# Optimization experiments

Hardware: AMD Instinct MI355X
Metric: run time of the kernel (lower is better)

The kernel has to match this reference:

```python
import jax, jax.numpy as jnp
import numpy as np

N = 100000      # nodes
E = 1600000     # edges (before self-loops)
F_IN = 128
H = 4           # heads, layer 1
C = 32          # hidden_size (per-head channels)
G = 256         # graphs in batch
NEG_SLOPE = 0.2 # PyG GATConv default


def setup_inputs() -> dict:
    key = jax.random.key(0)
    ks = jax.random.split(key, 12)
    x = jax.random.normal(ks[0], (N, F_IN), jnp.float32)
    edge_index = jax.random.randint(ks[1], (2, E), 0, N, dtype=jnp.int64)
    batch = jnp.sort(jax.random.randint(ks[2], (N,), 0, G, dtype=jnp.int64))
    s = lambda f: np.float32(1.0 / np.sqrt(f))
    W1 = jax.random.normal(ks[3], (F_IN, H * C), jnp.float32) * s(F_IN)
    att_src1 = jax.random.normal(ks[4], (H, C), jnp.float32) * 0.1
    att_dst1 = jax.random.normal(ks[5], (H, C), jnp.float32) * 0.1
    b1 = jnp.zeros((H * C,), jnp.float32)
    W2 = jax.random.normal(ks[6], (H * C, C), jnp.float32) * s(H * C)
    att_src2 = jax.random.normal(ks[7], (1, C), jnp.float32) * 0.1
    att_dst2 = jax.random.normal(ks[8], (1, C), jnp.float32) * 0.1
    b2 = jnp.zeros((C,), jnp.float32)
    Wfc = jax.random.normal(ks[9], (C, 1), jnp.float32) * s(C)
    bfc = jnp.zeros((1,), jnp.float32)
    return {"x": x, "edge_index": edge_index, "batch": batch,
            "W1": W1, "att_src1": att_src1, "att_dst1": att_dst1, "b1": b1,
            "W2": W2, "att_src2": att_src2, "att_dst2": att_dst2, "b2": b2,
            "Wfc": Wfc, "bfc": bfc}


def gat_conv(x, src, dst, W, att_s, att_d, b, heads, ch):
    """PyG GATConv (concat=True): linear, per-head additive attention,
    segment softmax over destination nodes, scatter-add aggregation."""
    n = x.shape[0]
    h = (x @ W).reshape(n, heads, ch)                         # [N,H,C]
    a_s = jnp.einsum('nhc,hc->nh', h, att_s)                  # [N,H]
    a_d = jnp.einsum('nhc,hc->nh', h, att_d)                  # [N,H]
    e = jax.nn.leaky_relu(a_s[src] + a_d[dst], NEG_SLOPE)     # [E,H]
    m = jax.ops.segment_max(e, dst, num_segments=n)           # stable softmax
    e = jnp.exp(e - m[dst])
    denom = jax.ops.segment_sum(e, dst, num_segments=n)
    alpha = e / denom[dst]                                    # [E,H]
    out = jax.ops.segment_sum(h[src] * alpha[:, :, None], dst, num_segments=n)
    return out.reshape(n, heads * ch) + b


def reference(x, edge_index, batch, W1, att_src1, att_dst1, b1,
              W2, att_src2, att_dst2, b2, Wfc, bfc):
    n = x.shape[0]
    loops = jnp.arange(n, dtype=edge_index.dtype)             # PyG add_self_loops=True
    src = jnp.concatenate([edge_index[0], loops])
    dst = jnp.concatenate([edge_index[1], loops])
    h = jax.nn.relu(gat_conv(x, src, dst, W1, att_src1, att_dst1, b1, H, C))
    h = jax.nn.relu(gat_conv(h, src, dst, W2, att_src2, att_dst2, b2, 1, C))
    # global_mean_pool over ragged graph segments
    sums = jax.ops.segment_sum(h, batch, num_segments=G)      # [G,C]
    cnts = jax.ops.segment_sum(jnp.ones((n,), h.dtype), batch, num_segments=G)
    pooled = sums / jnp.maximum(cnts, 1.0)[:, None]
    return (pooled @ Wfc + bfc).squeeze(-1)                   # [G]
```

## Files before the change

### kernel.cpp

```cpp
#include <hip/hip_runtime.h>
#include <cmath>

#define NEG_SLOPE 0.2f
#define DPB 128
#define EPB 4096

typedef unsigned int uint32;
typedef unsigned short ushort16;
typedef unsigned char uchar8;
typedef __attribute__((ext_vector_type(8))) short bf16x8;
typedef __attribute__((ext_vector_type(4))) float f32x4;
typedef __attribute__((ext_vector_type(2))) float f32x2;

__device__ __forceinline__ ushort16 f2bf(float x) {
    uint32 b = __float_as_uint(x);
    b += 0x7FFFu + ((b >> 16) & 1u);
    return (ushort16)(b >> 16);
}
__device__ __forceinline__ float bf2f_lo(uint32 u) { return __uint_as_float(u << 16); }
__device__ __forceinline__ float bf2f_hi(uint32 u) { return __uint_as_float(u & 0xFFFF0000u); }

__global__ void prep_B1(const float* __restrict__ W1, const float* __restrict__ atts,
                        const float* __restrict__ attd, ushort16* __restrict__ Bt) {
    int idx = blockIdx.x * 256 + threadIdx.x;
    if (idx >= 144 * 128) return;
    int n = idx >> 7, k = idx & 127;
    float v = 0.f;
    if (n < 128) v = W1[k * 128 + n];
    else if (n < 132) { int h = n - 128; for (int c = 0; c < 32; c++) v += W1[k*128 + h*32 + c] * atts[h*32 + c]; }
    else if (n < 136) { int h = n - 132; for (int c = 0; c < 32; c++) v += W1[k*128 + h*32 + c] * attd[h*32 + c]; }
    Bt[idx] = f2bf(v);
}
__global__ void prep_B2(const float* __restrict__ W2, const float* __restrict__ atts,
                        const float* __restrict__ attd, ushort16* __restrict__ Bt) {
    int idx = blockIdx.x * 256 + threadIdx.x;
    if (idx >= 48 * 128) return;
    int n = idx >> 7, k = idx & 127;
    float v = 0.f;
    if (n < 32) v = W2[k * 32 + n];
    else if (n == 32) { for (int c = 0; c < 32; c++) v += W2[k*32 + c] * atts[c]; }
    else if (n == 33) { for (int c = 0; c < 32; c++) v += W2[k*32 + c] * attd[c]; }
    Bt[idx] = f2bf(v);
}

template<int NT, int NH, bool XBF, bool OUT8>
__global__ __launch_bounds__(256) void gemm_mfma(
    const void* __restrict__ Xv, const ushort16* __restrict__ Bt,
    void* __restrict__ Houtv, float* __restrict__ asd, int M)
{
    constexpr int HT = NT - 1;
    constexpr int KP = 136;
    __shared__ ushort16 Bl[NT * 16 * KP];
    const int t = threadIdx.x;
    for (int i = t; i < NT * 16 * 32; i += 256) {
        int n = i >> 5, k4 = i & 31;
        uint2 v = *(const uint2*)&Bt[n * 128 + k4 * 4];
        *(uint2*)&Bl[n * KP + k4 * 4] = v;
    }
    __syncthreads();
    const int wave = t >> 6, lane = t & 63;
    const int lrow = lane & 15, lgrp = lane >> 4;
    const int ntiles = (M + 127) >> 7;
    const float* Xf = (const float*)Xv;
    const ushort16* Xb = (const ushort16*)Xv;

    for (int tile = blockIdx.x; tile < ntiles; tile += gridDim.x) {
        const int rbase = tile * 128 + wave * 32;
        f32x4 acc[2][NT];
        #pragma unroll
        for (int rs = 0; rs < 2; rs++)
            #pragma unroll
            for (int n = 0; n < NT; n++) acc[rs][n] = (f32x4){0.f, 0.f, 0.f, 0.f};

        for (int kk = 0; kk < 4; kk++) {
            bf16x8 bf[NT];
            #pragma unroll
            for (int n = 0; n < NT; n++)
                bf[n] = *(const bf16x8*)&Bl[(n * 16 + lrow) * KP + kk * 32 + lgrp * 8];
            #pragma unroll
            for (int rs = 0; rs < 2; rs++) {
                int row = rbase + rs * 16 + lrow;
                int rowc = row < M ? row : M - 1;
                bf16x8 af;
                if constexpr (XBF) {
                    af = *(const bf16x8*)&Xb[(long)rowc * 128 + kk * 32 + lgrp * 8];
                } else {
                    const float* xp = Xf + (long)rowc * 128 + kk * 32 + lgrp * 8;
                    float4 f0 = *(const float4*)xp;
                    float4 f1 = *(const float4*)(xp + 4);
                    union { uint32 u[4]; bf16x8 v; } pk;
                    pk.u[0] = (uint32)f2bf(f0.x) | ((uint32)f2bf(f0.y) << 16);
                    pk.u[1] = (uint32)f2bf(f0.z) | ((uint32)f2bf(f0.w) << 16);
                    pk.u[2] = (uint32)f2bf(f1.x) | ((uint32)f2bf(f1.y) << 16);
                    pk.u[3] = (uint32)f2bf(f1.z) | ((uint32)f2bf(f1.w) << 16);
                    af = pk.v;
                }
                #pragma unroll
                for (int n = 0; n < NT; n++)
                    acc[rs][n] = __builtin_amdgcn_mfma_f32_16x16x32_bf16(af, bf[n], acc[rs][n], 0, 0, 0);
            }
        }
        #pragma unroll
        for (int rs = 0; rs < 2; rs++) {
            #pragma unroll
            for (int r = 0; r < 4; r++) {
                const int row = rbase + rs * 16 + lgrp * 4 + r;
                if (row < M) {
                    if constexpr (OUT8) {
                        uchar8* H8 = (uchar8*)Houtv;
                        #pragma unroll
                        for (int n = 0; n < HT; n++) {
                            int pk = __builtin_amdgcn_cvt_pk_fp8_f32(acc[rs][n][r], 0.f, 0, false);
                            H8[(long)row * (HT * 16) + n * 16 + lrow] = (uchar8)pk;
                        }
                    } else {
                        ushort16* Hh = (ushort16*)Houtv;
                        #pragma unroll
                        for (int n = 0; n < HT; n++)
                            Hh[(long)row * (HT * 16) + n * 16 + lrow] = f2bf(acc[rs][n][r]);
                    }
                    if (lrow < 2 * NH)
                        asd[(long)row * (2 * NH) + lrow] = acc[rs][NT - 1][r];
                }
            }
        }
    }
}

__global__ __launch_bounds__(256) void buck_hist_k(
    const int* __restrict__ ei, int E, int Etot,
    int* __restrict__ cnt_bb, int NBUK_, int NBLK_)
{
    __shared__ int hist[1024];
    const int b = blockIdx.x, t = threadIdx.x;
    for (int i = t; i < NBUK_; i += 256) hist[i] = 0;
    __syncthreads();
    const int e0 = b * EPB;
    for (int i = t; i < EPB; i += 256) {
        int e = e0 + i;
        if (e < Etot) {
            int d = (e < E) ? ei[E + e] : (e - E);
            atomicAdd(&hist[d >> 7], 1);
        }
    }
    __syncthreads();
    for (int i = t; i < NBUK_; i += 256) cnt_bb[(size_t)i * NBLK_ + b] = hist[i];
}

__global__ __launch_bounds__(256) void buck_scan_row_k(
    int* __restrict__ cnt_bb, int* __restrict__ rowTot, int NBLK_)
{
    __shared__ int tmp[256];
    const int k = blockIdx.x, t = threadIdx.x;
    int* row = cnt_bb + (size_t)k * NBLK_;
    const int base = t * 4;
    int v[4]; int s = 0;
    #pragma unroll
    for (int j = 0; j < 4; j++) { v[j] = (base + j < NBLK_) ? row[base + j] : 0; s += v[j]; }
    tmp[t] = s; __syncthreads();
    for (int off = 1; off < 256; off <<= 1) {
        int x = (t >= off) ? tmp[t - off] : 0;
        __syncthreads();
        tmp[t] += x;
        __syncthreads();
    }
    int run = tmp[t] - s;
    if (t == 255) rowTot[k] = tmp[255];
    #pragma unroll
    for (int j = 0; j < 4; j++) { if (base + j < NBLK_) row[base + j] = run; run += v[j]; }
}

__global__ __launch_bounds__(256) void buck_base_k(
    const int* __restrict__ rowTot, int* __restrict__ bucketBase, int NBUK_)
{
    __shared__ int tmp[256];
    const int t = threadIdx.x;
    const int base = t * 4;
    int v[4]; int s = 0;
    #pragma unroll
    for (int j = 0; j < 4; j++) {
        v[j] = (base + j < NBUK_) ? ((rowTot[base + j] + 3 * DPB + 7) & ~7) : 0;
        s += v[j];
    }
    tmp[t] = s; __syncthreads();
    for (int off = 1; off < 256; off <<= 1) {
        int x = (t >= off) ? tmp[t - off] : 0;
        __syncthreads();
        tmp[t] += x;
        __syncthreads();
    }
    int run = tmp[t] - s;
    #pragma unroll
    for (int j = 0; j < 4; j++) { if (base + j < NBUK_) bucketBase[base + j] = run; run += v[j]; }
}

__global__ __launch_bounds__(256) void buck_scatter_k(
    const int* __restrict__ ei, int E, int Etot,
    const int* __restrict__ cnt_bb, const int* __restrict__ bucketBase,
    uint32* __restrict__ be, int NBUK_, int NBLK_)
{
    __shared__ int cur[1024];
    const int b = blockIdx.x, t = threadIdx.x;
    for (int i = t; i < NBUK_; i += 256)
        cur[i] = bucketBase[i] + cnt_bb[(size_t)i * NBLK_ + b];
    __syncthreads();
    const int e0 = b * EPB;
    for (int i = t; i < EPB; i += 256) {
        int e = e0 + i;
        if (e < Etot) {
            int srcv, d;
            if (e < E) { srcv = ei[e]; d = ei[E + e]; } else { srcv = d = e - E; }
            int slot = atomicAdd(&cur[d >> 7], 1);
            be[slot] = (uint32)srcv | ((uint32)(d & (DPB - 1)) << 20);
        }
    }
}

__global__ __launch_bounds__(256) void buck_finalize_k(
    const uint32* __restrict__ be, const int* __restrict__ rowTot,
    const int* __restrict__ bucketBase,
    int* __restrict__ csr, int* __restrict__ indptr, int* __restrict__ count, int N_)
{
    __shared__ int lhist[DPB];
    __shared__ int lptr[DPB];
    __shared__ int lcur[DPB];
    __shared__ int stmp[DPB];
    __shared__ int img[6144];
    __shared__ int paddedTotS;
    const int k = blockIdx.x, t = threadIdx.x;
    const int baseG = bucketBase[k];
    const int Mk = rowTot[k];
    if (t < DPB) lhist[t] = 0;
    __syncthreads();
    for (int i = t; i < Mk; i += 256) atomicAdd(&lhist[be[baseG + i] >> 20], 1);
    __syncthreads();
    int myp = (t < DPB) ? ((lhist[t] + 3) & ~3) : 0;
    if (t < DPB) stmp[t] = myp;
    __syncthreads();
    for (int off = 1; off < DPB; off <<= 1) {
        int x = (t < DPB && t >= off) ? stmp[t - off] : 0;
        __syncthreads();
        if (t < DPB) stmp[t] += x;
        __syncthreads();
    }
    if (t < DPB) { lptr[t] = stmp[t] - myp; lcur[t] = stmp[t] - myp; }
    if (t == DPB - 1) paddedTotS = stmp[t];
    __syncthreads();
    const int paddedTot = paddedTotS < 6144 ? paddedTotS : 6144;
    for (int i = t; i < paddedTot; i += 256) img[i] = 0;
    if (t < DPB) {
        int d = k * DPB + t;
        if (d < N_) { count[d] = lhist[t]; indptr[d] = baseG + lptr[t]; }
    }
    __syncthreads();
    for (int i = t; i < Mk; i += 256) {
        uint32 pk = be[baseG + i];
        int slot = atomicAdd(&lcur[pk >> 20], 1);
        if (slot < 6144) img[slot] = (int)(pk & 0xFFFFFu);
    }
    __syncthreads();
    for (int i = t; i < paddedTot; i += 256) csr[baseG + i] = img[i];
}

__global__ __launch_bounds__(256) void edge_p_k(
    const int* __restrict__ csr, const int* __restrict__ indptr, const int* __restrict__ count,
    const float* __restrict__ asd, ushort16* __restrict__ p1h, int N, int EP)
{
    int wave = threadIdx.x >> 6, lane = threadIdx.x & 63;
    int dst = blockIdx.x * 4 + wave;
    if (dst >= N) return;
    const char* asdb = (const char*)asd;
    const int start = indptr[dst], cnt = count[dst];
    const int cntp = (cnt + 3) & ~3;
    const float4 ad = *(const float4*)(asdb + (((uint32)dst << 5) | 16u));
    for (int k = lane; k < cntp; k += 64) {
        ushort16 r0 = 0, r1 = 0, r2 = 0, r3 = 0;
        if (k < cnt) {
            uint32 s = (uint32)csr[start + k];
            float4 as = *(const float4*)(asdb + (s << 5));
            float e0 = as.x + ad.x, e1 = as.y + ad.y, e2 = as.z + ad.z, e3 = as.w + ad.w;
            e0 = e0 >= 0.f ? e0 : NEG_SLOPE * e0;
            e1 = e1 >= 0.f ? e1 : NEG_SLOPE * e1;
            e2 = e2 >= 0.f ? e2 : NEG_SLOPE * e2;
            e3 = e3 >= 0.f ? e3 : NEG_SLOPE * e3;
            r0 = f2bf(__expf(e0)); r1 = f2bf(__expf(e1));
            r2 = f2bf(__expf(e2)); r3 = f2bf(__expf(e3));
        }
        const int pos = start + k;
        p1h[pos] = r0;
        p1h[EP + pos] = r1;
        p1h[2 * EP + pos] = r2;
        p1h[3 * EP + pos] = r3;
    }
}

__global__ __launch_bounds__(256) void edge_p2_k(
    const int* __restrict__ csr, const int* __restrict__ indptr, const int* __restrict__ count,
    const float* __restrict__ asd2, ushort16* __restrict__ p2, int N)
{
    int wave = threadIdx.x >> 6, lane = threadIdx.x & 63;
    int dst = blockIdx.x * 4 + wave;
    if (dst >= N) return;
    const char* asdb = (const char*)asd2;
    const int start = indptr[dst], cnt = count[dst];
    const int cntp = (cnt + 3) & ~3;
    const float ad = *(const float*)(asdb + (((uint32)dst << 3) | 4u));
    for (int k = lane; k < cntp; k += 64) {
        ushort16 r = 0;
        if (k < cnt) {
            uint32 s = (uint32)csr[start + k];
            float el = *(const float*)(asdb + (s << 3)) + ad;
            el = el >= 0.f ? el : NEG_SLOPE * el;
            r = f2bf(__expf(el));
        }
        p2[start + k] = r;
    }
}

__global__ __launch_bounds__(256) void agg_flash_h4(
    const int* __restrict__ csr, const ushort16* __restrict__ p1h,
    const int* __restrict__ indptr, const int* __restrict__ count,
    const uchar8* __restrict__ H8, const float* __restrict__ b1,
    uint32* __restrict__ Out, int N, int EP)
{
    int wave = threadIdx.x >> 6, lane = threadIdx.x & 63;
    int dst = blockIdx.x * 4 + wave;
    if (dst >= N) return;
    const char* Hb = (const char*)H8;
    const int head = lane >> 4;
    const uint32 ch2 = (uint32)(lane * 2);
    const int start = indptr[dst], cnt = count[dst];
    const int cntp = (cnt + 3) & ~3;
    const ushort16* pp = p1h + (size_t)head * EP + start;
    float s = 0.f, a0 = 0.f, a1 = 0.f;
    int k = 0;
    for (; k + 8 <= cntp; k += 8) {
        const int4 svA = *(const int4*)&csr[start + k];
        const int4 svB = *(const int4*)&csr[start + k + 4];
        const uint2 pwA = *(const uint2*)&pp[k];
        const uint2 pwB = *(const uint2*)&pp[k + 4];
        const uint32 u0 = *(const ushort16*)(Hb + (((uint32)svA.x << 7) | ch2));
        const uint32 u1 = *(const ushort16*)(Hb + (((uint32)svA.y << 7) | ch2));
        const uint32 u2 = *(const ushort16*)(Hb + (((uint32)svA.z << 7) | ch2));
        const uint32 u3 = *(const ushort16*)(Hb + (((uint32)svA.w << 7) | ch2));
        const uint32 u4 = *(const ushort16*)(Hb + (((uint32)svB.x << 7) | ch2));
        const uint32 u5 = *(const ushort16*)(Hb + (((uint32)svB.y << 7) | ch2));
        const uint32 u6 = *(const ushort16*)(Hb + (((uint32)svB.z << 7) | ch2));
        const uint32 u7 = *(const ushort16*)(Hb + (((uint32)svB.w << 7) | ch2));
        const f32x2 h0 = __builtin_amdgcn_cvt_pk_f32_fp8((int)u0, false);
        const f32x2 h1 = __builtin_amdgcn_cvt_pk_f32_fp8((int)u1, false);
        const f32x2 h2 = __builtin_amdgcn_cvt_pk_f32_fp8((int)u2, false);
        const f32x2 h3 = __builtin_amdgcn_cvt_pk_f32_fp8((int)u3, false);
        const f32x2 h4 = __builtin_amdgcn_cvt_pk_f32_fp8((int)u4, false);
        const f32x2 h5 = __builtin_amdgcn_cvt_pk_f32_fp8((int)u5, false);
        const f32x2 h6 = __builtin_amdgcn_cvt_pk_f32_fp8((int)u6, false);
        const f32x2 h7 = __builtin_amdgcn_cvt_pk_f32_fp8((int)u7, false);
        const float p0 = bf2f_lo(pwA.x), p1v = bf2f_hi(pwA.x);
        const float p2v = bf2f_lo(pwA.y), p3v = bf2f_hi(pwA.y);
        const float p4v = bf2f_lo(pwB.x), p5v = bf2f_hi(pwB.x);
        const float p6v = bf2f_lo(pwB.y), p7v = bf2f_hi(pwB.y);
        s += ((p0 + p1v) + (p2v + p3v)) + ((p4v + p5v) + (p6v + p7v));
        a0 += p0 * h0[0];  a1 += p0 * h0[1];
        a0 += p1v * h1[0]; a1 += p1v * h1[1];
        a0 += p2v * h2[0]; a1 += p2v * h2[1];
        a0 += p3v * h3[0]; a1 += p3v * h3[1];
        a0 += p4v * h4[0]; a1 += p4v * h4[1];
        a0 += p5v * h5[0]; a1 += p5v * h5[1];
        a0 += p6v * h6[0]; a1 += p6v * h6[1];
        a0 += p7v * h7[0]; a1 += p7v * h7[1];
    }
    if (k < cntp) {
        const int4 sv = *(const int4*)&csr[start + k];
        const uint2 pw = *(const uint2*)&pp[k];
        const uint32 u0 = *(const ushort16*)(Hb + (((uint32)sv.x << 7) | ch2));
        const uint32 u1 = *(const ushort16*)(Hb + (((uint32)sv.y << 7) | ch2));
        const uint32 u2 = *(const ushort16*)(Hb + (((uint32)sv.z << 7) | ch2));
        const uint32 u3 = *(const ushort16*)(Hb + (((uint32)sv.w << 7) | ch2));
        const f32x2 h0 = __builtin_amdgcn_cvt_pk_f32_fp8((int)u0, false);
        const f32x2 h1 = __builtin_amdgcn_cvt_pk_f32_fp8((int)u1, false);
        const f32x2 h2 = __builtin_amdgcn_cvt_pk_f32_fp8((int)u2, false);
        const f32x2 h3 = __builtin_amdgcn_cvt_pk_f32_fp8((int)u3, false);
        const float p0 = bf2f_lo(pw.x), p1v = bf2f_hi(pw.x);
        const float p2v = bf2f_lo(pw.y), p3v = bf2f_hi(pw.y);
        s += (p0 + p1v) + (p2v + p3v);
        a0 += p0 * h0[0];  a1 += p0 * h0[1];
        a0 += p1v * h1[0]; a1 += p1v * h1[1];
        a0 += p2v * h2[0]; a1 += p2v * h2[1];
        a0 += p3v * h3[0]; a1 += p3v * h3[1];
    }
    const float inv = 1.f / s;
    const float2 bb = *(const float2*)&b1[ch2];
    float o0 = fmaxf(a0 * inv + bb.x, 0.f);
    float o1 = fmaxf(a1 * inv + bb.y, 0.f);
    Out[(long)dst * 64 + lane] = (uint32)f2bf(o0) | ((uint32)f2bf(o1) << 16);
}

__global__ __launch_bounds__(256) void agg_flash_h1(
    const int* __restrict__ csr, const ushort16* __restrict__ p2,
    const int* __restrict__ indptr, const int* __restrict__ count,
    const uchar8* __restrict__ H8, float* __restrict__ Out, int N)
{
    int wave = threadIdx.x >> 6, lane = threadIdx.x & 63;
    int dst = blockIdx.x * 4 + wave;
    if (dst >= N) return;
    const char* Hb = (const char*)H8;
    const int c2 = lane & 15, grp = lane >> 4;
    const uint32 cb = (uint32)(c2 * 2);
    const int start = indptr[dst];
    const int cntp = (count[dst] + 3) & ~3;
    float s = 0.f, a0 = 0.f, a1 = 0.f;
    for (int k = grp * 4; k < cntp; k += 16) {
        const int4  sv = *(const int4*)&csr[start + k];
        const uint2 pv = *(const uint2*)&p2[start + k];
        const uint32 u0 = *(const ushort16*)(Hb + (((uint32)sv.x << 5) | cb));
        const uint32 u1 = *(const ushort16*)(Hb + (((uint32)sv.y << 5) | cb));
        const uint32 u2 = *(const ushort16*)(Hb + (((uint32)sv.z << 5) | cb));
        const uint32 u3 = *(const ushort16*)(Hb + (((uint32)sv.w << 5) | cb));
        const f32x2 h0 = __builtin_amdgcn_cvt_pk_f32_fp8((int)u0, false);
        const f32x2 h1 = __builtin_amdgcn_cvt_pk_f32_fp8((int)u1, false);
        const f32x2 h2 = __builtin_amdgcn_cvt_pk_f32_fp8((int)u2, false);
        const f32x2 h3 = __builtin_amdgcn_cvt_pk_f32_fp8((int)u3, false);
        float q0 = bf2f_lo(pv.x), q1 = bf2f_hi(pv.x);
        float q2 = bf2f_lo(pv.y), q3 = bf2f_hi(pv.y);
        s += (q0 + q1) + (q2 + q3);
        a0 += q0 * h0[0]; a1 += q0 * h0[1];
        a0 += q1 * h1[0]; a1 += q1 * h1[1];
        a0 += q2 * h2[0]; a1 += q2 * h2[1];
        a0 += q3 * h3[0]; a1 += q3 * h3[1];
    }
    s  += __shfl_xor(s, 16, 64);  s  += __shfl_xor(s, 32, 64);
    a0 += __shfl_xor(a0, 16, 64); a0 += __shfl_xor(a0, 32, 64);
    a1 += __shfl_xor(a1, 16, 64); a1 += __shfl_xor(a1, 32, 64);
    if (grp == 0) {
        const float inv = 1.f / s;
        float2 o; o.x = a0 * inv; o.y = a1 * inv;
        *(float2*)&Out[(long)dst * 32 + c2 * 2] = o;
    }
}

__global__ __launch_bounds__(256) void pool_fc_kernel(
    const float* __restrict__ Agg2, const float* __restrict__ b2,
    const int* __restrict__ batch,
    const float* __restrict__ Wfc, const float* __restrict__ bfc,
    float* __restrict__ out, int N)
{
    __shared__ float part[8][32];
    const int g = blockIdx.x;
    const int t = threadIdx.x;
    const int c = t & 31, grp = t >> 5;

    int lo = 0, hi = N;
    while (lo < hi) { int mid = (lo + hi) >> 1; if (batch[mid] < g) lo = mid + 1; else hi = mid; }
    const int start = lo;
    hi = N;
    while (lo < hi) { int mid = (lo + hi) >> 1; if (batch[mid] <= g) lo = mid + 1; else hi = mid; }
    const int end = lo;

    const float bc = b2[c];
    float acc = 0.f;
    for (int i = start + grp; i < end; i += 8)
        acc += fmaxf(Agg2[(long)i * 32 + c] + bc, 0.f);
    part[grp][c] = acc;
    __syncthreads();
    if (t < 32) {
        float s = 0.f;
        #pragma unroll
        for (int r = 0; r < 8; r++) s += part[r][c];
        const float cnt = fmaxf((float)(end - start), 1.f);
        float v = (s / cnt) * Wfc[c];
        #pragma unroll
        for (int m = 16; m >= 1; m >>= 1) v += __shfl_xor(v, m, 64);
        if (c == 0) out[g] = v + bfc[0];
    }
}

extern "C" void kernel_launch(void* const* d_in, const int* in_sizes, int n_in,
                              void* d_out, int out_size, void* d_ws, size_t ws_size,
                              hipStream_t stream)
{
    const float* x     = (const float*)d_in[0];
    const int*   ei    = (const int*)d_in[1];
    const int*   batch = (const int*)d_in[2];
    const float* W1    = (const float*)d_in[3];
    const float* atts1 = (const float*)d_in[4];
    const float* attd1 = (const float*)d_in[5];
    const float* b1    = (const float*)d_in[6];
    const float* W2    = (const float*)d_in[7];
    const float* atts2 = (const float*)d_in[8];
    const float* attd2 = (const float*)d_in[9];
    const float* b2    = (const float*)d_in[10];
    const float* Wfc   = (const float*)d_in[11];
    const float* bfc   = (const float*)d_in[12];
    float* out = (float*)d_out;

    const int N = in_sizes[0] / 128;
    const int E = in_sizes[1] / 2;
    const int Etot = E + N;
    const int G = out_size;
    const int NBUK = (N + DPB - 1) / DPB;
    const int NBLK = (Etot + EPB - 1) / EPB;
    const int CSRCAP = (Etot + NBUK * (3 * DPB + 8) + 7) & ~7;
    const int ntiles = (N + 127) >> 7;

    float* w = (float*)d_ws;
    uchar8* h1   = (uchar8*)w; w += (size_t)N * 32;
    uchar8* h2   = (uchar8*)w; w += (size_t)N * 8;
    uint32* agg1 = (uint32*)w; w += (size_t)N * 64;
    float* agg2 = w; w += (size_t)N * 32;
    float* asd1 = w; w += (size_t)N * 8;
    float* asd2 = w; w += (size_t)N * 2;
    ushort16* Bt1 = (ushort16*)w; w += (144 * 128) / 2;
    ushort16* Bt2 = (ushort16*)w; w += (48 * 128) / 2;
    int* count  = (int*)w; w += N;
    int* indptr = (int*)w; w += N;
    int* cnt_bb = (int*)w; w += (size_t)NBUK * NBLK;
    int* rowTot = (int*)w; w += NBUK;
    int* bucketBase = (int*)w; w += NBUK;
    uint32* be  = (uint32*)w; w += CSRCAP;
    int* csr    = (int*)w; w += CSRCAP;
    ushort16* p1h = (ushort16*)w; w += (size_t)CSRCAP * 2;
    ushort16* p2  = (ushort16*)w; w += CSRCAP / 2;

    prep_B1<<<(144 * 128 + 255) / 256, 256, 0, stream>>>(W1, atts1, attd1, Bt1);
    prep_B2<<<(48 * 128 + 255) / 256, 256, 0, stream>>>(W2, atts2, attd2, Bt2);

    gemm_mfma<9, 4, false, true><<<ntiles, 256, 0, stream>>>(x, Bt1, h1, asd1, N);

    buck_hist_k<<<NBLK, 256, 0, stream>>>(ei, E, Etot, cnt_bb, NBUK, NBLK);
    buck_scan_row_k<<<NBUK, 256, 0, stream>>>(cnt_bb, rowTot, NBLK);
    buck_base_k<<<1, 256, 0, stream>>>(rowTot, bucketBase, NBUK);
    buck_scatter_k<<<NBLK, 256, 0, stream>>>(ei, E, Etot, cnt_bb, bucketBase, be, NBUK, NBLK);
    buck_finalize_k<<<NBUK, 256, 0, stream>>>(be, rowTot, bucketBase, csr, indptr, count, N);

    edge_p_k<<<(N + 3) / 4, 256, 0, stream>>>(csr, indptr, count, asd1, p1h, N, CSRCAP);
    agg_flash_h4<<<(N + 3) / 4, 256, 0, stream>>>(csr, p1h, indptr, count, h1, b1, agg1, N, CSRCAP);

    gemm_mfma<3, 1, true, true><<<ntiles, 256, 0, stream>>>(agg1, Bt2, h2, asd2, N);
    edge_p2_k<<<(N + 3) / 4, 256, 0, stream>>>(csr, indptr, count, asd2, p2, N);
    agg_flash_h1<<<(N + 3) / 4, 256, 0, stream>>>(csr, p2, indptr, count, h2, agg2, N);

    pool_fc_kernel<<<G, 256, 0, stream>>>(agg2, b2, batch, Wfc, bfc, out, N);
}
```

Before: 242.2 us.

## Pre-shift CSR indices, pad rows to 8, widen aggregation loads to 4 fp8 channels

The CSR entries now store the source index already shifted to a byte offset, so the gathers no longer need a per-edge shift. Per-destination padding goes from 4 to 8 so both aggregation kernels can split each row's edges across two lane halves (h4) or eight groups (h1). Each lane now loads 4 fp8 channels per gather instead of 2, halving the number of gather instructions, and the partial sums are combined with a cross-lane reduction. The two weight-prep kernels are also merged into one launch. In exchange the padding overhead and CSR capacity grow, and the h4 kernel gains a cross-lane reduction step.

```diff
diff --git a/kernel.cpp b/kernel.cpp
--- a/kernel.cpp
+++ b/kernel.cpp
@@ -20,27 +20,29 @@
 __device__ __forceinline__ float bf2f_lo(uint32 u) { return __uint_as_float(u << 16); }
 __device__ __forceinline__ float bf2f_hi(uint32 u) { return __uint_as_float(u & 0xFFFF0000u); }
 
-__global__ void prep_B1(const float* __restrict__ W1, const float* __restrict__ atts,
-                        const float* __restrict__ attd, ushort16* __restrict__ Bt) {
+__global__ void prep_B(const float* __restrict__ W1, const float* __restrict__ atts1,
+                       const float* __restrict__ attd1,
+                       const float* __restrict__ W2, const float* __restrict__ atts2,
+                       const float* __restrict__ attd2,
+                       ushort16* __restrict__ Bt1, ushort16* __restrict__ Bt2) {
     int idx = blockIdx.x * 256 + threadIdx.x;
-    if (idx >= 144 * 128) return;
-    int n = idx >> 7, k = idx & 127;
-    float v = 0.f;
-    if (n < 128) v = W1[k * 128 + n];
-    else if (n < 132) { int h = n - 128; for (int c = 0; c < 32; c++) v += W1[k*128 + h*32 + c] * atts[h*32 + c]; }
-    else if (n < 136) { int h = n - 132; for (int c = 0; c < 32; c++) v += W1[k*128 + h*32 + c] * attd[h*32 + c]; }
-    Bt[idx] = f2bf(v);
-}
-__global__ void prep_B2(const float* __restrict__ W2, const float* __restrict__ atts,
-                        const float* __restrict__ attd, ushort16* __restrict__ Bt) {
-    int idx = blockIdx.x * 256 + threadIdx.x;
-    if (idx >= 48 * 128) return;
-    int n = idx >> 7, k = idx & 127;
-    float v = 0.f;
-    if (n < 32) v = W2[k * 32 + n];
-    else if (n == 32) { for (int c = 0; c < 32; c++) v += W2[k*32 + c] * atts[c]; }
-    else if (n == 33) { for (int c = 0; c < 32; c++) v += W2[k*32 + c] * attd[c]; }
-    Bt[idx] = f2bf(v);
+    if (idx < 144 * 128) {
+        int n = idx >> 7, k = idx & 127;
+        float v = 0.f;
+        if (n < 128) v = W1[k * 128 + n];
+        else if (n < 132) { int h = n - 128; for (int c = 0; c < 32; c++) v += W1[k*128 + h*32 + c] * atts1[h*32 + c]; }
+        else if (n < 136) { int h = n - 132; for (int c = 0; c < 32; c++) v += W1[k*128 + h*32 + c] * attd1[h*32 + c]; }
+        Bt1[idx] = f2bf(v);
+    } else {
+        int j = idx - 144 * 128;
+        if (j >= 48 * 128) return;
+        int n = j >> 7, k = j & 127;
+        float v = 0.f;
+        if (n < 32) v = W2[k * 32 + n];
+        else if (n == 32) { for (int c = 0; c < 32; c++) v += W2[k*32 + c] * atts2[c]; }
+        else if (n == 33) { for (int c = 0; c < 32; c++) v += W2[k*32 + c] * attd2[c]; }
+        Bt2[j] = f2bf(v);
+    }
 }
 
 template<int NT, int NH, bool XBF, bool OUT8>
@@ -179,7 +181,7 @@
     int v[4]; int s = 0;
     #pragma unroll
     for (int j = 0; j < 4; j++) {
-        v[j] = (base + j < NBUK_) ? ((rowTot[base + j] + 3 * DPB + 7) & ~7) : 0;
+        v[j] = (base + j < NBUK_) ? ((rowTot[base + j] + 7 * DPB + 7) & ~7) : 0;
         s += v[j];
     }
     tmp[t] = s; __syncthreads();
@@ -234,7 +236,7 @@
     __syncthreads();
     for (int i = t; i < Mk; i += 256) atomicAdd(&lhist[be[baseG + i] >> 20], 1);
     __syncthreads();
-    int myp = (t < DPB) ? ((lhist[t] + 3) & ~3) : 0;
+    int myp = (t < DPB) ? ((lhist[t] + 7) & ~7) : 0;
     if (t < DPB) stmp[t] = myp;
     __syncthreads();
     for (int off = 1; off < DPB; off <<= 1) {
@@ -256,7 +258,7 @@
     for (int i = t; i < Mk; i += 256) {
         uint32 pk = be[baseG + i];
         int slot = atomicAdd(&lcur[pk >> 20], 1);
-        if (slot < 6144) img[slot] = (int)(pk & 0xFFFFFu);
+        if (slot < 6144) img[slot] = (int)((pk & 0xFFFFFu) << 7);
     }
     __syncthreads();
     for (int i = t; i < paddedTot; i += 256) csr[baseG + i] = img[i];
@@ -271,13 +273,13 @@
     if (dst >= N) return;
     const char* asdb = (const char*)asd;
     const int start = indptr[dst], cnt = count[dst];
-    const int cntp = (cnt + 3) & ~3;
+    const int cntp = (cnt + 7) & ~7;
     const float4 ad = *(const float4*)(asdb + (((uint32)dst << 5) | 16u));
     for (int k = lane; k < cntp; k += 64) {
         ushort16 r0 = 0, r1 = 0, r2 = 0, r3 = 0;
         if (k < cnt) {
-            uint32 s = (uint32)csr[start + k];
-            float4 as = *(const float4*)(asdb + (s << 5));
+            uint32 sb = (uint32)csr[start + k];
+            float4 as = *(const float4*)(asdb + (sb >> 2));
             float e0 = as.x + ad.x, e1 = as.y + ad.y, e2 = as.z + ad.z, e3 = as.w + ad.w;
             e0 = e0 >= 0.f ? e0 : NEG_SLOPE * e0;
             e1 = e1 >= 0.f ? e1 : NEG_SLOPE * e1;
@@ -303,13 +305,13 @@
     if (dst >= N) return;
     const char* asdb = (const char*)asd2;
     const int start = indptr[dst], cnt = count[dst];
-    const int cntp = (cnt + 3) & ~3;
+    const int cntp = (cnt + 7) & ~7;
     const float ad = *(const float*)(asdb + (((uint32)dst << 3) | 4u));
     for (int k = lane; k < cntp; k += 64) {
         ushort16 r = 0;
         if (k < cnt) {
-            uint32 s = (uint32)csr[start + k];
-            float el = *(const float*)(asdb + (s << 3)) + ad;
+            uint32 sb = (uint32)csr[start + k];
+            float el = *(const float*)(asdb + (sb >> 4)) + ad;
             el = el >= 0.f ? el : NEG_SLOPE * el;
             r = f2bf(__expf(el));
         }
@@ -327,72 +329,54 @@
     int dst = blockIdx.x * 4 + wave;
     if (dst >= N) return;
     const char* Hb = (const char*)H8;
-    const int head = lane >> 4;
-    const uint32 ch2 = (uint32)(lane * 2);
+    const int l32 = lane & 31, half = lane >> 5;
+    const int head = l32 >> 3;
+    const uint32 cb = (uint32)(l32 * 4);
     const int start = indptr[dst], cnt = count[dst];
-    const int cntp = (cnt + 3) & ~3;
-    const ushort16* pp = p1h + (size_t)head * EP + start;
-    float s = 0.f, a0 = 0.f, a1 = 0.f;
-    int k = 0;
-    for (; k + 8 <= cntp; k += 8) {
-        const int4 svA = *(const int4*)&csr[start + k];
-        const int4 svB = *(const int4*)&csr[start + k + 4];
-        const uint2 pwA = *(const uint2*)&pp[k];
-        const uint2 pwB = *(const uint2*)&pp[k + 4];
-        const uint32 u0 = *(const ushort16*)(Hb + (((uint32)svA.x << 7) | ch2));
-        const uint32 u1 = *(const ushort16*)(Hb + (((uint32)svA.y << 7) | ch2));
-        const uint32 u2 = *(const ushort16*)(Hb + (((uint32)svA.z << 7) | ch2));
-        const uint32 u3 = *(const ushort16*)(Hb + (((uint32)svA.w << 7) | ch2));
-        const uint32 u4 = *(const ushort16*)(Hb + (((uint32)svB.x << 7) | ch2));
-        const uint32 u5 = *(const ushort16*)(Hb + (((uint32)svB.y << 7) | ch2));
-        const uint32 u6 = *(const ushort16*)(Hb + (((uint32)svB.z << 7) | ch2));
-        const uint32 u7 = *(const ushort16*)(Hb + (((uint32)svB.w << 7) | ch2));
-        const f32x2 h0 = __builtin_amdgcn_cvt_pk_f32_fp8((int)u0, false);
-        const f32x2 h1 = __builtin_amdgcn_cvt_pk_f32_fp8((int)u1, false);
-        const f32x2 h2 = __builtin_amdgcn_cvt_pk_f32_fp8((int)u2, false);
-        const f32x2 h3 = __builtin_amdgcn_cvt_pk_f32_fp8((int)u3, false);
-        const f32x2 h4 = __builtin_amdgcn_cvt_pk_f32_fp8((int)u4, false);
-        const f32x2 h5 = __builtin_amdgcn_cvt_pk_f32_fp8((int)u5, false);
-        const f32x2 h6 = __builtin_amdgcn_cvt_pk_f32_fp8((int)u6, false);
-        const f32x2 h7 = __builtin_amdgcn_cvt_pk_f32_fp8((int)u7, false);
-        const float p0 = bf2f_lo(pwA.x), p1v = bf2f_hi(pwA.x);
-        const float p2v = bf2f_lo(pwA.y), p3v = bf2f_hi(pwA.y);
-        const float p4v = bf2f_lo(pwB.x), p5v = bf2f_hi(pwB.x);
-        const float p6v = bf2f_lo(pwB.y), p7v = bf2f_hi(pwB.y);
-        s += ((p0 + p1v) + (p2v + p3v)) + ((p4v + p5v) + (p6v + p7v));
-        a0 += p0 * h0[0];  a1 += p0 * h0[1];
-        a0 += p1v * h1[0]; a1 += p1v * h1[1];
-        a0 += p2v * h2[0]; a1 += p2v * h2[1];
-        a0 += p3v * h3[0]; a1 += p3v * h3[1];
-        a0 += p4v * h4[0]; a1 += p4v * h4[1];
-        a0 += p5v * h5[0]; a1 += p5v * h5[1];
-        a0 += p6v * h6[0]; a1 += p6v * h6[1];
-        a0 += p7v * h7[0]; a1 += p7v * h7[1];
-    }
-    if (k < cntp) {
-        const int4 sv = *(const int4*)&csr[start + k];
+    const int cntp = (cnt + 7) & ~7;
+    const int* cp = csr + start + half * 4;
+    const ushort16* pp = p1h + (size_t)head * EP + start + half * 4;
+    float s = 0.f, a0 = 0.f, a1 = 0.f, a2 = 0.f, a3 = 0.f;
+    for (int k = 0; k < cntp; k += 8) {
+        const int4 sv = *(const int4*)&cp[k];
         const uint2 pw = *(const uint2*)&pp[k];
-        const uint32 u0 = *(const ushort16*)(Hb + (((uint32)sv.x << 7) | ch2));
-        const uint32 u1 = *(const ushort16*)(Hb + (((uint32)sv.y << 7) | ch2));
-        const uint32 u2 = *(const ushort16*)(Hb + (((uint32)sv.z << 7) | ch2));
-        const uint32 u3 = *(const ushort16*)(Hb + (((uint32)sv.w << 7) | ch2));
-        const f32x2 h0 = __builtin_amdgcn_cvt_pk_f32_fp8((int)u0, false);
-        const f32x2 h1 = __builtin_amdgcn_cvt_pk_f32_fp8((int)u1, false);
-        const f32x2 h2 = __builtin_amdgcn_cvt_pk_f32_fp8((int)u2, false);
-        const f32x2 h3 = __builtin_amdgcn_cvt_pk_f32_fp8((int)u3, false);
+        const uint32 u0 = *(const uint32*)(Hb + ((uint32)sv.x | cb));
+        const uint32 u1 = *(const uint32*)(Hb + ((uint32)sv.y | cb));
+        const uint32 u2 = *(const uint32*)(Hb + ((uint32)sv.z | cb));
+        const uint32 u3 = *(const uint32*)(Hb + ((uint32)sv.w | cb));
+        const f32x2 l0 = __builtin_amdgcn_cvt_pk_f32_fp8((int)u0, false);
+        const f32x2 g0 = __builtin_amdgcn_cvt_pk_f32_fp8((int)u0, true);
+        const f32x2 l1 = __builtin_amdgcn_cvt_pk_f32_fp8((int)u1, false);
+        const f32x2 g1 = __builtin_amdgcn_cvt_pk_f32_fp8((int)u1, true);
+        const f32x2 l2 = __builtin_amdgcn_cvt_pk_f32_fp8((int)u2, false);
+        const f32x2 g2 = __builtin_amdgcn_cvt_pk_f32_fp8((int)u2, true);
+        const f32x2 l3 = __builtin_amdgcn_cvt_pk_f32_fp8((int)u3, false);
+        const f32x2 g3 = __builtin_amdgcn_cvt_pk_f32_fp8((int)u3, true);
         const float p0 = bf2f_lo(pw.x), p1v = bf2f_hi(pw.x);
         const float p2v = bf2f_lo(pw.y), p3v = bf2f_hi(pw.y);
         s += (p0 + p1v) + (p2v + p3v);
-        a0 += p0 * h0[0];  a1 += p0 * h0[1];
-        a0 += p1v * h1[0]; a1 += p1v * h1[1];
-        a0 += p2v * h2[0]; a1 += p2v * h2[1];
-        a0 += p3v * h3[0]; a1 += p3v * h3[1];
-    }
-    const float inv = 1.f / s;
-    const float2 bb = *(const float2*)&b1[ch2];
-    float o0 = fmaxf(a0 * inv + bb.x, 0.f);
-    float o1 = fmaxf(a1 * inv + bb.y, 0.f);
-    Out[(long)dst * 64 + lane] = (uint32)f2bf(o0) | ((uint32)f2bf(o1) << 16);
+        a0 += p0 * l0[0];  a1 += p0 * l0[1];  a2 += p0 * g0[0];  a3 += p0 * g0[1];
+        a0 += p1v * l1[0]; a1 += p1v * l1[1]; a2 += p1v * g1[0]; a3 += p1v * g1[1];
+        a0 += p2v * l2[0]; a1 += p2v * l2[1]; a2 += p2v * g2[0]; a3 += p2v * g2[1];
+        a0 += p3v * l3[0]; a1 += p3v * l3[1]; a2 += p3v * g3[0]; a3 += p3v * g3[1];
+    }
+    s  += __shfl_xor(s, 32, 64);
+    a0 += __shfl_xor(a0, 32, 64);
+    a1 += __shfl_xor(a1, 32, 64);
+    a2 += __shfl_xor(a2, 32, 64);
+    a3 += __shfl_xor(a3, 32, 64);
+    if (half == 0) {
+        const float inv = 1.f / s;
+        const float4 bb = *(const float4*)&b1[l32 * 4];
+        float o0 = fmaxf(a0 * inv + bb.x, 0.f);
+        float o1 = fmaxf(a1 * inv + bb.y, 0.f);
+        float o2 = fmaxf(a2 * inv + bb.z, 0.f);
+        float o3 = fmaxf(a3 * inv + bb.w, 0.f);
+        uint2 o;
+        o.x = (uint32)f2bf(o0) | ((uint32)f2bf(o1) << 16);
+        o.y = (uint32)f2bf(o2) | ((uint32)f2bf(o3) << 16);
+        *(uint2*)&Out[(long)dst * 64 + l32 * 2] = o;
+    }
 }
 
 __global__ __launch_bounds__(256) void agg_flash_h1(
@@ -404,37 +388,46 @@
     int dst = blockIdx.x * 4 + wave;
     if (dst >= N) return;
     const char* Hb = (const char*)H8;
-    const int c2 = lane & 15, grp = lane >> 4;
-    const uint32 cb = (uint32)(c2 * 2);
+    const int c4 = lane & 7, grp = lane >> 3;
+    const uint32 cb = (uint32)(c4 * 4);
     const int start = indptr[dst];
-    const int cntp = (count[dst] + 3) & ~3;
-    float s = 0.f, a0 = 0.f, a1 = 0.f;
-    for (int k = grp * 4; k < cntp; k += 16) {
+    const int cntp = (count[dst] + 7) & ~7;
+    float s = 0.f, a0 = 0.f, a1 = 0.f, a2 = 0.f, a3 = 0.f;
+    for (int k = grp * 4; k < cntp; k += 32) {
         const int4  sv = *(const int4*)&csr[start + k];
         const uint2 pv = *(const uint2*)&p2[start + k];
-        const uint32 u0 = *(const ushort16*)(Hb + (((uint32)sv.x << 5) | cb));
-        const uint32 u1 = *(const ushort16*)(Hb + (((uint32)sv.y << 5) | cb));
-        const uint32 u2 = *(const ushort16*)(Hb + (((uint32)sv.z << 5) | cb));
-        const uint32 u3 = *(const ushort16*)(Hb + (((uint32)sv.w << 5) | cb));
-        const f32x2 h0 = __builtin_amdgcn_cvt_pk_f32_fp8((int)u0, false);
-        const f32x2 h1 = __builtin_amdgcn_cvt_pk_f32_fp8((int)u1, false);
-        const f32x2 h2 = __builtin_amdgcn_cvt_pk_f32_fp8((int)u2, false);
-        const f32x2 h3 = __builtin_amdgcn_cvt_pk_f32_fp8((int)u3, false);
+        const uint32 u0 = *(const uint32*)(Hb + (((uint32)sv.x >> 2) | cb));
+        const uint32 u1 = *(const uint32*)(Hb + (((uint32)sv.y >> 2) | cb));
+        const uint32 u2 = *(const uint32*)(Hb + (((uint32)sv.z >> 2) | cb));
+        const uint32 u3 = *(const uint32*)(Hb + (((uint32)sv.w >> 2) | cb));
+        const f32x2 l0 = __builtin_amdgcn_cvt_pk_f32_fp8((int)u0, false);
+        const f32x2 g0 = __builtin_amdgcn_cvt_pk_f32_fp8((int)u0, true);
+        const f32x2 l1 = __builtin_amdgcn_cvt_pk_f32_fp8((int)u1, false);
+        const f32x2 g1 = __builtin_amdgcn_cvt_pk_f32_fp8((int)u1, true);
+        const f32x2 l2 = __builtin_amdgcn_cvt_pk_f32_fp8((int)u2, false);
+        const f32x2 g2 = __builtin_amdgcn_cvt_pk_f32_fp8((int)u2, true);
+        const f32x2 l3 = __builtin_amdgcn_cvt_pk_f32_fp8((int)u3, false);
+        const f32x2 g3 = __builtin_amdgcn_cvt_pk_f32_fp8((int)u3, true);
         float q0 = bf2f_lo(pv.x), q1 = bf2f_hi(pv.x);
         float q2 = bf2f_lo(pv.y), q3 = bf2f_hi(pv.y);
         s += (q0 + q1) + (q2 + q3);
-        a0 += q0 * h0[0]; a1 += q0 * h0[1];
-        a0 += q1 * h1[0]; a1 += q1 * h1[1];
-        a0 += q2 * h2[0]; a1 += q2 * h2[1];
-        a0 += q3 * h3[0]; a1 += q3 * h3[1];
-    }
-    s  += __shfl_xor(s, 16, 64);  s  += __shfl_xor(s, 32, 64);
-    a0 += __shfl_xor(a0, 16, 64); a0 += __shfl_xor(a0, 32, 64);
-    a1 += __shfl_xor(a1, 16, 64); a1 += __shfl_xor(a1, 32, 64);
+        a0 += q0 * l0[0]; a1 += q0 * l0[1]; a2 += q0 * g0[0]; a3 += q0 * g0[1];
+        a0 += q1 * l1[0]; a1 += q1 * l1[1]; a2 += q1 * g1[0]; a3 += q1 * g1[1];
+        a0 += q2 * l2[0]; a1 += q2 * l2[1]; a2 += q2 * g2[0]; a3 += q2 * g2[1];
+        a0 += q3 * l3[0]; a1 += q3 * l3[1]; a2 += q3 * g3[0]; a3 += q3 * g3[1];
+    }
+    #pragma unroll
+    for (int m = 8; m <= 32; m <<= 1) {
+        s  += __shfl_xor(s, m, 64);
+        a0 += __shfl_xor(a0, m, 64);
+        a1 += __shfl_xor(a1, m, 64);
+        a2 += __shfl_xor(a2, m, 64);
+        a3 += __shfl_xor(a3, m, 64);
+    }
     if (grp == 0) {
         const float inv = 1.f / s;
-        float2 o; o.x = a0 * inv; o.y = a1 * inv;
-        *(float2*)&Out[(long)dst * 32 + c2 * 2] = o;
+        float4 o; o.x = a0 * inv; o.y = a1 * inv; o.z = a2 * inv; o.w = a3 * inv;
+        *(float4*)&Out[(long)dst * 32 + c4 * 4] = o;
     }
 }
 
@@ -499,7 +492,7 @@
     const int G = out_size;
     const int NBUK = (N + DPB - 1) / DPB;
     const int NBLK = (Etot + EPB - 1) / EPB;
-    const int CSRCAP = (Etot + NBUK * (3 * DPB + 8) + 7) & ~7;
+    const int CSRCAP = (Etot + NBUK * (7 * DPB + 8) + 7) & ~7;
     const int ntiles = (N + 127) >> 7;
 
     float* w = (float*)d_ws;
@@ -521,8 +514,7 @@
     ushort16* p1h = (ushort16*)w; w += (size_t)CSRCAP * 2;
     ushort16* p2  = (ushort16*)w; w += CSRCAP / 2;
 
-    prep_B1<<<(144 * 128 + 255) / 256, 256, 0, stream>>>(W1, atts1, attd1, Bt1);
-    prep_B2<<<(48 * 128 + 255) / 256, 256, 0, stream>>>(W2, atts2, attd2, Bt2);
+    prep_B<<<(192 * 128 + 255) / 256, 256, 0, stream>>>(W1, atts1, attd1, W2, atts2, attd2, Bt1, Bt2);
 
     gemm_mfma<9, 4, false, true><<<ntiles, 256, 0, stream>>>(x, Bt1, h1, asd1, N);
 
```

Measured after the change: 238.9 us. No clear change (-1.4%).

## Fuse layer-1 edge score computation into CSR finalize and pre-scale CSR indices

Applied to the files above, without the earlier changes.

Merges the two weight-prep kernels into one launch, and folds the layer-1 edge attention/exp computation into the bucket finalize kernel. The finalize kernel now keeps the destination of each slot in shared memory and caches the destination attention values, which removes a separate pass that re-read the CSR. CSR entries are stored pre-shifted (source index << 7) so the gather kernels skip a shift when forming addresses and use a right shift instead. This adds shared-memory use in finalize, which may lower occupancy, and limits how large source indices can be before the shifted value overflows.

```diff
diff --git a/kernel.cpp b/kernel.cpp
--- a/kernel.cpp
+++ b/kernel.cpp
@@ -20,27 +20,29 @@
 __device__ __forceinline__ float bf2f_lo(uint32 u) { return __uint_as_float(u << 16); }
 __device__ __forceinline__ float bf2f_hi(uint32 u) { return __uint_as_float(u & 0xFFFF0000u); }
 
-__global__ void prep_B1(const float* __restrict__ W1, const float* __restrict__ atts,
-                        const float* __restrict__ attd, ushort16* __restrict__ Bt) {
+__global__ void prep_B(const float* __restrict__ W1, const float* __restrict__ atts1,
+                       const float* __restrict__ attd1,
+                       const float* __restrict__ W2, const float* __restrict__ atts2,
+                       const float* __restrict__ attd2,
+                       ushort16* __restrict__ Bt1, ushort16* __restrict__ Bt2) {
     int idx = blockIdx.x * 256 + threadIdx.x;
-    if (idx >= 144 * 128) return;
-    int n = idx >> 7, k = idx & 127;
-    float v = 0.f;
-    if (n < 128) v = W1[k * 128 + n];
-    else if (n < 132) { int h = n - 128; for (int c = 0; c < 32; c++) v += W1[k*128 + h*32 + c] * atts[h*32 + c]; }
-    else if (n < 136) { int h = n - 132; for (int c = 0; c < 32; c++) v += W1[k*128 + h*32 + c] * attd[h*32 + c]; }
-    Bt[idx] = f2bf(v);
-}
-__global__ void prep_B2(const float* __restrict__ W2, const float* __restrict__ atts,
-                        const float* __restrict__ attd, ushort16* __restrict__ Bt) {
-    int idx = blockIdx.x * 256 + threadIdx.x;
-    if (idx >= 48 * 128) return;
-    int n = idx >> 7, k = idx & 127;
-    float v = 0.f;
-    if (n < 32) v = W2[k * 32 + n];
-    else if (n == 32) { for (int c = 0; c < 32; c++) v += W2[k*32 + c] * atts[c]; }
-    else if (n == 33) { for (int c = 0; c < 32; c++) v += W2[k*32 + c] * attd[c]; }
-    Bt[idx] = f2bf(v);
+    if (idx < 144 * 128) {
+        int n = idx >> 7, k = idx & 127;
+        float v = 0.f;
+        if (n < 128) v = W1[k * 128 + n];
+        else if (n < 132) { int h = n - 128; for (int c = 0; c < 32; c++) v += W1[k*128 + h*32 + c] * atts1[h*32 + c]; }
+        else if (n < 136) { int h = n - 132; for (int c = 0; c < 32; c++) v += W1[k*128 + h*32 + c] * attd1[h*32 + c]; }
+        Bt1[idx] = f2bf(v);
+    } else {
+        int j = idx - 144 * 128;
+        if (j >= 48 * 128) return;
+        int n = j >> 7, k = j & 127;
+        float v = 0.f;
+        if (n < 32) v = W2[k * 32 + n];
+        else if (n == 32) { for (int c = 0; c < 32; c++) v += W2[k*32 + c] * atts2[c]; }
+        else if (n == 33) { for (int c = 0; c < 32; c++) v += W2[k*32 + c] * attd2[c]; }
+        Bt2[j] = f2bf(v);
+    }
 }
 
 template<int NT, int NH, bool XBF, bool OUT8>
@@ -218,14 +220,17 @@
 
 __global__ __launch_bounds__(256) void buck_finalize_k(
     const uint32* __restrict__ be, const int* __restrict__ rowTot,
-    const int* __restrict__ bucketBase,
-    int* __restrict__ csr, int* __restrict__ indptr, int* __restrict__ count, int N_)
+    const int* __restrict__ bucketBase, const float* __restrict__ asd1,
+    int* __restrict__ csr, int* __restrict__ indptr, int* __restrict__ count,
+    ushort16* __restrict__ p1h, int N_, int EP)
 {
     __shared__ int lhist[DPB];
     __shared__ int lptr[DPB];
     __shared__ int lcur[DPB];
     __shared__ int stmp[DPB];
     __shared__ int img[6144];
+    __shared__ short slot2d[6144];
+    __shared__ float4 adl[DPB];
     __shared__ int paddedTotS;
     const int k = blockIdx.x, t = threadIdx.x;
     const int baseG = bucketBase[k];
@@ -247,37 +252,35 @@
     if (t == DPB - 1) paddedTotS = stmp[t];
     __syncthreads();
     const int paddedTot = paddedTotS < 6144 ? paddedTotS : 6144;
-    for (int i = t; i < paddedTot; i += 256) img[i] = 0;
+    for (int i = t; i < paddedTot; i += 256) { img[i] = 0; slot2d[i] = -1; }
     if (t < DPB) {
         int d = k * DPB + t;
-        if (d < N_) { count[d] = lhist[t]; indptr[d] = baseG + lptr[t]; }
+        if (d < N_) {
+            count[d] = lhist[t];
+            indptr[d] = baseG + lptr[t];
+            adl[t] = *(const float4*)&asd1[(size_t)d * 8 + 4];
+        }
     }
     __syncthreads();
     for (int i = t; i < Mk; i += 256) {
         uint32 pk = be[baseG + i];
-        int slot = atomicAdd(&lcur[pk >> 20], 1);
-        if (slot < 6144) img[slot] = (int)(pk & 0xFFFFFu);
-    }
-    __syncthreads();
-    for (int i = t; i < paddedTot; i += 256) csr[baseG + i] = img[i];
-}
-
-__global__ __launch_bounds__(256) void edge_p_k(
-    const int* __restrict__ csr, const int* __restrict__ indptr, const int* __restrict__ count,
-    const float* __restrict__ asd, ushort16* __restrict__ p1h, int N, int EP)
-{
-    int wave = threadIdx.x >> 6, lane = threadIdx.x & 63;
-    int dst = blockIdx.x * 4 + wave;
-    if (dst >= N) return;
-    const char* asdb = (const char*)asd;
-    const int start = indptr[dst], cnt = count[dst];
-    const int cntp = (cnt + 3) & ~3;
-    const float4 ad = *(const float4*)(asdb + (((uint32)dst << 5) | 16u));
-    for (int k = lane; k < cntp; k += 64) {
+        int dloc = (int)(pk >> 20);
+        int slot = atomicAdd(&lcur[dloc], 1);
+        if (slot < 6144) {
+            img[slot] = (int)((pk & 0xFFFFFu) << 7);
+            slot2d[slot] = (short)dloc;
+        }
+    }
+    __syncthreads();
+    const char* asdb = (const char*)asd1;
+    for (int i = t; i < paddedTot; i += 256) {
+        const int sb = img[i];
+        csr[baseG + i] = sb;
+        const int dloc = slot2d[i];
         ushort16 r0 = 0, r1 = 0, r2 = 0, r3 = 0;
-        if (k < cnt) {
-            uint32 s = (uint32)csr[start + k];
-            float4 as = *(const float4*)(asdb + (s << 5));
+        if (dloc >= 0) {
+            float4 as = *(const float4*)(asdb + (((uint32)sb) >> 2));
+            float4 ad = adl[dloc];
             float e0 = as.x + ad.x, e1 = as.y + ad.y, e2 = as.z + ad.z, e3 = as.w + ad.w;
             e0 = e0 >= 0.f ? e0 : NEG_SLOPE * e0;
             e1 = e1 >= 0.f ? e1 : NEG_SLOPE * e1;
@@ -286,7 +289,7 @@
             r0 = f2bf(__expf(e0)); r1 = f2bf(__expf(e1));
             r2 = f2bf(__expf(e2)); r3 = f2bf(__expf(e3));
         }
-        const int pos = start + k;
+        const int pos = baseG + i;
         p1h[pos] = r0;
         p1h[EP + pos] = r1;
         p1h[2 * EP + pos] = r2;
@@ -308,8 +311,8 @@
     for (int k = lane; k < cntp; k += 64) {
         ushort16 r = 0;
         if (k < cnt) {
-            uint32 s = (uint32)csr[start + k];
-            float el = *(const float*)(asdb + (s << 3)) + ad;
+            uint32 sb = (uint32)csr[start + k];
+            float el = *(const float*)(asdb + (sb >> 4)) + ad;
             el = el >= 0.f ? el : NEG_SLOPE * el;
             r = f2bf(__expf(el));
         }
@@ -339,14 +342,14 @@
         const int4 svB = *(const int4*)&csr[start + k + 4];
         const uint2 pwA = *(const uint2*)&pp[k];
         const uint2 pwB = *(const uint2*)&pp[k + 4];
-        const uint32 u0 = *(const ushort16*)(Hb + (((uint32)svA.x << 7) | ch2));
-        const uint32 u1 = *(const ushort16*)(Hb + (((uint32)svA.y << 7) | ch2));
-        const uint32 u2 = *(const ushort16*)(Hb + (((uint32)svA.z << 7) | ch2));
-        const uint32 u3 = *(const ushort16*)(Hb + (((uint32)svA.w << 7) | ch2));
-        const uint32 u4 = *(const ushort16*)(Hb + (((uint32)svB.x << 7) | ch2));
-        const uint32 u5 = *(const ushort16*)(Hb + (((uint32)svB.y << 7) | ch2));
-        const uint32 u6 = *(const ushort16*)(Hb + (((uint32)svB.z << 7) | ch2));
-        const uint32 u7 = *(const ushort16*)(Hb + (((uint32)svB.w << 7) | ch2));
+        const uint32 u0 = *(const ushort16*)(Hb + ((uint32)svA.x | ch2));
+        const uint32 u1 = *(const ushort16*)(Hb + ((uint32)svA.y | ch2));
+        const uint32 u2 = *(const ushort16*)(Hb + ((uint32)svA.z | ch2));
+        const uint32 u3 = *(const ushort16*)(Hb + ((uint32)svA.w | ch2));
+        const uint32 u4 = *(const ushort16*)(Hb + ((uint32)svB.x | ch2));
+        const uint32 u5 = *(const ushort16*)(Hb + ((uint32)svB.y | ch2));
+        const uint32 u6 = *(const ushort16*)(Hb + ((uint32)svB.z | ch2));
+        const uint32 u7 = *(const ushort16*)(Hb + ((uint32)svB.w | ch2));
         const f32x2 h0 = __builtin_amdgcn_cvt_pk_f32_fp8((int)u0, false);
         const f32x2 h1 = __builtin_amdgcn_cvt_pk_f32_fp8((int)u1, false);
         const f32x2 h2 = __builtin_amdgcn_cvt_pk_f32_fp8((int)u2, false);
@@ -372,10 +375,10 @@
     if (k < cntp) {
         const int4 sv = *(const int4*)&csr[start + k];
         const uint2 pw = *(const uint2*)&pp[k];
-        const uint32 u0 = *(const ushort16*)(Hb + (((uint32)sv.x << 7) | ch2));
-        const uint32 u1 = *(const ushort16*)(Hb + (((uint32)sv.y << 7) | ch2));
-        const uint32 u2 = *(const ushort16*)(Hb + (((uint32)sv.z << 7) | ch2));
-        const uint32 u3 = *(const ushort16*)(Hb + (((uint32)sv.w << 7) | ch2));
+        const uint32 u0 = *(const ushort16*)(Hb + ((uint32)sv.x | ch2));
+        const uint32 u1 = *(const ushort16*)(Hb + ((uint32)sv.y | ch2));
+        const uint32 u2 = *(const ushort16*)(Hb + ((uint32)sv.z | ch2));
+        const uint32 u3 = *(const ushort16*)(Hb + ((uint32)sv.w | ch2));
         const f32x2 h0 = __builtin_amdgcn_cvt_pk_f32_fp8((int)u0, false);
         const f32x2 h1 = __builtin_amdgcn_cvt_pk_f32_fp8((int)u1, false);
         const f32x2 h2 = __builtin_amdgcn_cvt_pk_f32_fp8((int)u2, false);
@@ -412,10 +415,10 @@
     for (int k = grp * 4; k < cntp; k += 16) {
         const int4  sv = *(const int4*)&csr[start + k];
         const uint2 pv = *(const uint2*)&p2[start + k];
-        const uint32 u0 = *(const ushort16*)(Hb + (((uint32)sv.x << 5) | cb));
-        const uint32 u1 = *(const ushort16*)(Hb + (((uint32)sv.y << 5) | cb));
-        const uint32 u2 = *(const ushort16*)(Hb + (((uint32)sv.z << 5) | cb));
-        const uint32 u3 = *(const ushort16*)(Hb + (((uint32)sv.w << 5) | cb));
+        const uint32 u0 = *(const ushort16*)(Hb + (((uint32)sv.x >> 2) | cb));
+        const uint32 u1 = *(const ushort16*)(Hb + (((uint32)sv.y >> 2) | cb));
+        const uint32 u2 = *(const ushort16*)(Hb + (((uint32)sv.z >> 2) | cb));
+        const uint32 u3 = *(const ushort16*)(Hb + (((uint32)sv.w >> 2) | cb));
         const f32x2 h0 = __builtin_amdgcn_cvt_pk_f32_fp8((int)u0, false);
         const f32x2 h1 = __builtin_amdgcn_cvt_pk_f32_fp8((int)u1, false);
         const f32x2 h2 = __builtin_amdgcn_cvt_pk_f32_fp8((int)u2, false);
@@ -521,8 +524,7 @@
     ushort16* p1h = (ushort16*)w; w += (size_t)CSRCAP * 2;
     ushort16* p2  = (ushort16*)w; w += CSRCAP / 2;
 
-    prep_B1<<<(144 * 128 + 255) / 256, 256, 0, stream>>>(W1, atts1, attd1, Bt1);
-    prep_B2<<<(48 * 128 + 255) / 256, 256, 0, stream>>>(W2, atts2, attd2, Bt2);
+    prep_B<<<(192 * 128 + 255) / 256, 256, 0, stream>>>(W1, atts1, attd1, W2, atts2, attd2, Bt1, Bt2);
 
     gemm_mfma<9, 4, false, true><<<ntiles, 256, 0, stream>>>(x, Bt1, h1, asd1, N);
 
@@ -530,9 +532,9 @@
     buck_scan_row_k<<<NBUK, 256, 0, stream>>>(cnt_bb, rowTot, NBLK);
     buck_base_k<<<1, 256, 0, stream>>>(rowTot, bucketBase, NBUK);
     buck_scatter_k<<<NBLK, 256, 0, stream>>>(ei, E, Etot, cnt_bb, bucketBase, be, NBUK, NBLK);
-    buck_finalize_k<<<NBUK, 256, 0, stream>>>(be, rowTot, bucketBase, csr, indptr, count, N);
-
-    edge_p_k<<<(N + 3) / 4, 256, 0, stream>>>(csr, indptr, count, asd1, p1h, N, CSRCAP);
+    buck_finalize_k<<<NBUK, 256, 0, stream>>>(be, rowTot, bucketBase, asd1,
+                                              csr, indptr, count, p1h, N, CSRCAP);
+
     agg_flash_h4<<<(N + 3) / 4, 256, 0, stream>>>(csr, p1h, indptr, count, h1, b1, agg1, N, CSRCAP);
 
     gemm_mfma<3, 1, true, true><<<ntiles, 256, 0, stream>>>(agg1, Bt2, h2, asd2, N);
```

Result: faster. 231.1 us (median of 2 runs) (-4.6%).
